# Kernel tuning notes

Measured on AMD Instinct MI355X. Metric: run time of the kernel, lower is better.

Reference implementation:

```python
import jax, jax.numpy as jnp
import numpy as np

B, L, D, H = 2, 2048, 1024, 16
DK = D // H


def setup_inputs() -> dict:
    key = jax.random.key(0)
    ks = jax.random.split(key, 5)
    s = 1.0 / np.sqrt(D)
    query = jax.random.normal(ks[0], (B, L, D), dtype=jnp.float32)
    # causal mask, True = masked (masked_fill semantics), broadcastable to [B,H,L,L]
    mask = jnp.triu(jnp.ones((L, L), dtype=bool), k=1)[None, None, :, :]
    W_q = jax.random.normal(ks[1], (D, D), dtype=jnp.float32) * s
    W_k = jax.random.normal(ks[2], (D, D), dtype=jnp.float32) * s
    W_v = jax.random.normal(ks[3], (D, D), dtype=jnp.float32) * s
    W_o = jax.random.normal(ks[4], (D, D), dtype=jnp.float32) * s
    return {"query": query, "mask": mask, "W_q": W_q, "W_k": W_k, "W_v": W_v, "W_o": W_o}


def reference(query, mask, W_q, W_k, W_v, W_o):
    b, l, d = query.shape
    # projections (torch Linear with bias=False; weights here stored as [in,out])
    q = (query @ W_q).reshape(b, l, H, DK).transpose(0, 2, 1, 3)  # [B,H,L,dk]
    k = (query @ W_k).reshape(b, l, H, DK).transpose(0, 2, 1, 3)
    v = (query @ W_v).reshape(b, l, H, DK).transpose(0, 2, 1, 3)
    scores = jnp.einsum("bhqd,bhkd->bhqk", q, k) / np.sqrt(DK)  # [B,H,L,L]
    scores = jnp.where(mask, jnp.asarray(-1e9, scores.dtype), scores)
    A = jax.nn.softmax(scores, axis=-1)  # [B,H,L,L]
    out = jnp.einsum("bhqk,bhkd->bhqd", A, v)  # [B,H,L,dk]
    out = out.transpose(0, 2, 1, 3).reshape(b, l, d)  # [B,L,D]
    y = out @ W_o
    return (y, A)
```

## Files before the change

kernel.cpp:

```cpp
#include <hip/hip_runtime.h>


typedef _Float16 h8 __attribute__((ext_vector_type(8)));
typedef _Float16 h4 __attribute__((ext_vector_type(4)));
typedef float f4 __attribute__((ext_vector_type(4)));

#define L_SEQ 2048
#define NH 16
#define DKH 64
#define DM 1024

static __device__ __forceinline__ void gload16(const void* g, void* l) {
  __builtin_amdgcn_global_load_lds(
      (const __attribute__((address_space(1))) char*)g,
      (__attribute__((address_space(3))) char*)l, 16, 0, 0);
}

__global__ __launch_bounds__(256) void k_cast(const float* __restrict__ in,
                                              _Float16* __restrict__ out, int n4) {
  int i = blockIdx.x * 256 + threadIdx.x;
  if (i >= n4) return;
  f4 v = ((const f4*)in)[i];
  h4 o = {(_Float16)v[0], (_Float16)v[1], (_Float16)v[2], (_Float16)v[3]};
  ((h4*)out)[i] = o;
}

__global__ __launch_bounds__(256) void k_wt(const float* w0, const float* w1,
                                            const float* w2, const float* w3,
                                            _Float16* o0, _Float16* o1,
                                            _Float16* o2, _Float16* o3) {
  __shared__ _Float16 tile[64][65];
  const float* W;
  _Float16* O;
  switch (blockIdx.z) {
    case 0: W = w0; O = o0; break;
    case 1: W = w1; O = o1; break;
    case 2: W = w2; O = o2; break;
    default: W = w3; O = o3; break;
  }
  int n0 = blockIdx.x * 64, k0 = blockIdx.y * 64;
  int t = threadIdx.x, c = t & 63, r0 = (t >> 6) * 16;
  for (int i = 0; i < 16; ++i)
    tile[r0 + i][c] = (_Float16)W[(size_t)(k0 + r0 + i) * DM + n0 + c];
  __syncthreads();
  for (int i = 0; i < 16; ++i)
    O[(size_t)(n0 + r0 + i) * DM + k0 + c] = tile[c][r0 + i];
}

__global__ __launch_bounds__(256) void k_vt(const _Float16* __restrict__ Vb,
                                            _Float16* __restrict__ Vt) {
  __shared__ _Float16 tile[64][65];
  int blk = blockIdx.x, bh = blk >> 5, l0 = (blk & 31) * 64;
  const _Float16* src = Vb + (size_t)bh * L_SEQ * DKH;
  _Float16* dst = Vt + (size_t)bh * DKH * L_SEQ;
  int t = threadIdx.x, c = t & 63, r0 = (t >> 6) * 16;
  for (int i = 0; i < 16; ++i)
    tile[r0 + i][c] = src[(size_t)(l0 + r0 + i) * DKH + c];
  __syncthreads();
  for (int i = 0; i < 16; ++i)
    dst[(size_t)(r0 + i) * L_SEQ + l0 + c] = tile[c][r0 + i];
}

__global__ __launch_bounds__(256) void k_gemm(const _Float16* __restrict__ A,
                                              const _Float16* __restrict__ B0,
                                              const _Float16* __restrict__ B1,
                                              const _Float16* __restrict__ B2,
                                              void* o0, void* o1, void* o2,
                                              int mode) {
  const _Float16* Bt = blockIdx.z == 0 ? B0 : (blockIdx.z == 1 ? B1 : B2);
  void* out = blockIdx.z == 0 ? o0 : (blockIdx.z == 1 ? o1 : o2);
  __shared__ __align__(16) _Float16 lA[128 * 32];
  __shared__ __align__(16) _Float16 lB[128 * 32];
  int t = threadIdx.x, lane = t & 63, w = t >> 6;
  int l15 = lane & 15, g = lane >> 4;
  int wr = w >> 1, wc = w & 1;
  int m0 = blockIdx.x * 128, n0 = blockIdx.y * 128;
  f4 zed = {0.f, 0.f, 0.f, 0.f};
  f4 acc[4][4];
  for (int i = 0; i < 4; ++i)
    for (int j = 0; j < 4; ++j) acc[i][j] = zed;

  int row = t >> 2, colh = (t & 3) * 8;
  const _Float16* ga = A + (size_t)(m0 + row) * DM + colh;
  const _Float16* gb = Bt + (size_t)(n0 + row) * DM + colh;
  _Float16* la0 = &lA[row * 32 + colh];
  _Float16* la1 = &lA[2048 + row * 32 + colh];
  _Float16* lb0 = &lB[row * 32 + colh];
  _Float16* lb1 = &lB[2048 + row * 32 + colh];

  for (int k0 = 0; k0 < DM; k0 += 32) {
    __syncthreads();
    gload16(ga + k0, la0);
    gload16(ga + (size_t)64 * DM + k0, la1);
    gload16(gb + k0, lb0);
    gload16(gb + (size_t)64 * DM + k0, lb1);
    __syncthreads();
    h8 af[4], bfr[4];
#pragma unroll
    for (int mr = 0; mr < 4; ++mr)
      af[mr] = *(const h8*)&lA[(wr * 64 + mr * 16 + l15) * 32 + g * 8];
#pragma unroll
    for (int nr = 0; nr < 4; ++nr)
      bfr[nr] = *(const h8*)&lB[(wc * 64 + nr * 16 + l15) * 32 + g * 8];
#pragma unroll
    for (int mr = 0; mr < 4; ++mr)
#pragma unroll
      for (int nr = 0; nr < 4; ++nr)
        acc[mr][nr] = __builtin_amdgcn_mfma_f32_16x16x32_f16(af[mr], bfr[nr],
                                                             acc[mr][nr], 0, 0, 0);
  }

  if (mode == 0) {
    _Float16* o = (_Float16*)out;
#pragma unroll
    for (int mr = 0; mr < 4; ++mr)
#pragma unroll
      for (int nr = 0; nr < 4; ++nr) {
        int n = n0 + wc * 64 + nr * 16 + l15;
        int h = n >> 6, dk = n & 63;
#pragma unroll
        for (int r = 0; r < 4; ++r) {
          int m = m0 + wr * 64 + mr * 16 + g * 4 + r;
          int b = m >> 11, l = m & 2047;
          o[(((size_t)b * NH + h) * L_SEQ + l) * DKH + dk] = (_Float16)acc[mr][nr][r];
        }
      }
  } else {
    float* o = (float*)out;
#pragma unroll
    for (int mr = 0; mr < 4; ++mr)
#pragma unroll
      for (int nr = 0; nr < 4; ++nr) {
        int n = n0 + wc * 64 + nr * 16 + l15;
#pragma unroll
        for (int r = 0; r < 4; ++r) {
          int m = m0 + wr * 64 + mr * 16 + g * 4 + r;
          o[(size_t)m * DM + n] = acc[mr][nr][r];
        }
      }
  }
}

__global__ __launch_bounds__(256, 2) void k_attn(const _Float16* __restrict__ Qh,
                                                 const _Float16* __restrict__ Kh,
                                                 const _Float16* __restrict__ Vt,
                                                 float* __restrict__ Aout,
                                                 _Float16* __restrict__ Oh) {
  __shared__ __align__(16) _Float16 Plds[4][2][1024];
  const int blk = blockIdx.x;
  const int bh = blk & 31;
  const int qt = 15 - (blk >> 5);
  const int b = bh >> 4, h = bh & 15;
  const int t = threadIdx.x, w = t >> 6, lane = t & 63;
  const int l15 = lane & 15, g = lane >> 4;
  const int q0 = qt * 128 + w * 32;
  const int qa = q0 + l15;
  const int qb = q0 + 16 + l15;

  const _Float16* Qp = Qh + ((size_t)bh * L_SEQ + qa) * DKH + g * 8;
  const h8 qa0 = *(const h8*)Qp;
  const h8 qa1 = *(const h8*)(Qp + 32);
  const h8 qb0 = *(const h8*)(Qp + 16 * DKH);
  const h8 qb1 = *(const h8*)(Qp + 16 * DKH + 32);
  const _Float16* Kbase = Kh + (size_t)bh * L_SEQ * DKH;
  const _Float16* Vbase = Vt + (size_t)bh * DKH * L_SEQ;
  float* Abase = Aout + (size_t)bh * L_SEQ * L_SEQ;
  char* pA = (char*)&Plds[w][0][0];
  char* pB = (char*)&Plds[w][1][0];
  const int swz = (l15 & 7) << 4;

  const float SC = 0.125f * 1.44269504089f;
  const int nfull = q0 >> 6;
  f4 zed = {0.f, 0.f, 0.f, 0.f};

  float mA = -1e30f, sumA = 0.f, mB = -1e30f, sumB = 0.f;
  for (int c = 0; c < nfull; ++c) {
    const _Float16* Kp = Kbase + (size_t)(c * 64 + l15) * DKH + g * 8;
    h8 kf0[4], kf1[4];
#pragma unroll
    for (int tt = 0; tt < 4; ++tt) {
      kf0[tt] = *(const h8*)(Kp + (size_t)tt * 16 * DKH);
      kf1[tt] = *(const h8*)(Kp + (size_t)tt * 16 * DKH + 32);
    }
    f4 sa[4], sb[4];
    __builtin_amdgcn_s_setprio(1);
#pragma unroll
    for (int tt = 0; tt < 4; ++tt) {
      sa[tt] = __builtin_amdgcn_mfma_f32_16x16x32_f16(kf0[tt], qa0, zed, 0, 0, 0);
      sa[tt] = __builtin_amdgcn_mfma_f32_16x16x32_f16(kf1[tt], qa1, sa[tt], 0, 0, 0);
      sb[tt] = __builtin_amdgcn_mfma_f32_16x16x32_f16(kf0[tt], qb0, zed, 0, 0, 0);
      sb[tt] = __builtin_amdgcn_mfma_f32_16x16x32_f16(kf1[tt], qb1, sb[tt], 0, 0, 0);
    }
    __builtin_amdgcn_s_setprio(0);
#pragma unroll
    for (int tt = 0; tt < 4; ++tt)
#pragma unroll
      for (int r = 0; r < 4; ++r) {
        float va = sa[tt][r] * SC, vb = sb[tt][r] * SC;
        mA = fmaxf(mA, va);
        sumA += __builtin_amdgcn_exp2f(va);
        mB = fmaxf(mB, vb);
        sumB += __builtin_amdgcn_exp2f(vb);
      }
  }
  {
    const _Float16* Kp = Kbase + (size_t)(nfull * 64 + l15) * DKH + g * 8;
    h8 kf0[4], kf1[4];
#pragma unroll
    for (int tt = 0; tt < 4; ++tt) {
      kf0[tt] = *(const h8*)(Kp + (size_t)tt * 16 * DKH);
      kf1[tt] = *(const h8*)(Kp + (size_t)tt * 16 * DKH + 32);
    }
    f4 sa[4], sb[4];
    __builtin_amdgcn_s_setprio(1);
#pragma unroll
    for (int tt = 0; tt < 4; ++tt) {
      sa[tt] = __builtin_amdgcn_mfma_f32_16x16x32_f16(kf0[tt], qa0, zed, 0, 0, 0);
      sa[tt] = __builtin_amdgcn_mfma_f32_16x16x32_f16(kf1[tt], qa1, sa[tt], 0, 0, 0);
      sb[tt] = __builtin_amdgcn_mfma_f32_16x16x32_f16(kf0[tt], qb0, zed, 0, 0, 0);
      sb[tt] = __builtin_amdgcn_mfma_f32_16x16x32_f16(kf1[tt], qb1, sb[tt], 0, 0, 0);
    }
    __builtin_amdgcn_s_setprio(0);
#pragma unroll
    for (int tt = 0; tt < 4; ++tt) {
      int kb = nfull * 64 + tt * 16 + g * 4;
#pragma unroll
      for (int r = 0; r < 4; ++r) {
        float va = (kb + r <= qa) ? sa[tt][r] * SC : -1e30f;
        float vb = (kb + r <= qb) ? sb[tt][r] * SC : -1e30f;
        mA = fmaxf(mA, va);
        sumA += __builtin_amdgcn_exp2f(va);
        mB = fmaxf(mB, vb);
        sumB += __builtin_amdgcn_exp2f(vb);
      }
    }
  }
  mA = fmaxf(mA, __shfl_xor(mA, 16, 64));
  sumA += __shfl_xor(sumA, 16, 64);
  mA = fmaxf(mA, __shfl_xor(mA, 32, 64));
  sumA += __shfl_xor(sumA, 32, 64);
  mB = fmaxf(mB, __shfl_xor(mB, 16, 64));
  sumB += __shfl_xor(sumB, 16, 64);
  mB = fmaxf(mB, __shfl_xor(mB, 32, 64));
  sumB += __shfl_xor(sumB, 32, 64);
  const float cA = fmaxf(mA - 12.f, 0.f);
  const float cB = fmaxf(mB - 12.f, 0.f);
  const float invA = __builtin_amdgcn_exp2f(cA) / sumA;
  const float invB = __builtin_amdgcn_exp2f(cB) / sumB;

  f4 oaccA[4], oaccB[4];
#pragma unroll
  for (int dt = 0; dt < 4; ++dt) { oaccA[dt] = zed; oaccB[dt] = zed; }

  for (int cc = 0; cc <= nfull; ++cc) {
    const _Float16* Kp = Kbase + (size_t)(cc * 64 + l15) * DKH + g * 8;
    h8 kf0[4], kf1[4];
#pragma unroll
    for (int tt = 0; tt < 4; ++tt) {
      kf0[tt] = *(const h8*)(Kp + (size_t)tt * 16 * DKH);
      kf1[tt] = *(const h8*)(Kp + (size_t)tt * 16 * DKH + 32);
    }
    const _Float16* Vp = Vbase + (size_t)l15 * L_SEQ + cc * 64 + g * 8;
    h8 vf[8];
#pragma unroll
    for (int ks = 0; ks < 2; ++ks)
#pragma unroll
      for (int dt = 0; dt < 4; ++dt)
        vf[ks * 4 + dt] = *(const h8*)(Vp + (size_t)dt * 16 * L_SEQ + ks * 32);

    f4 sa[4], sb[4];
    __builtin_amdgcn_s_setprio(1);
#pragma unroll
    for (int tt = 0; tt < 4; ++tt) {
      sa[tt] = __builtin_amdgcn_mfma_f32_16x16x32_f16(kf0[tt], qa0, zed, 0, 0, 0);
      sa[tt] = __builtin_amdgcn_mfma_f32_16x16x32_f16(kf1[tt], qa1, sa[tt], 0, 0, 0);
      sb[tt] = __builtin_amdgcn_mfma_f32_16x16x32_f16(kf0[tt], qb0, zed, 0, 0, 0);
      sb[tt] = __builtin_amdgcn_mfma_f32_16x16x32_f16(kf1[tt], qb1, sb[tt], 0, 0, 0);
    }
    __builtin_amdgcn_s_setprio(0);

    const bool dchunk = (cc == nfull);
    float* ArowA = Abase + (size_t)qa * L_SEQ + cc * 64 + g * 4;
    float* ArowB = Abase + (size_t)qb * L_SEQ + cc * 64 + g * 4;
#pragma unroll
    for (int tt = 0; tt < 4; ++tt) {
      f4 pv;
#pragma unroll
      for (int r = 0; r < 4; ++r) {
        float sv = sa[tt][r] * SC - cA;
        if (dchunk && (cc * 64 + tt * 16 + g * 4 + r > qa)) sv = -1e30f;
        pv[r] = __builtin_amdgcn_exp2f(sv);
      }
      f4 av = {pv[0] * invA, pv[1] * invA, pv[2] * invA, pv[3] * invA};
      *(f4*)(ArowA + tt * 16) = av;
      h4 ph = {(_Float16)pv[0], (_Float16)pv[1], (_Float16)pv[2], (_Float16)pv[3]};
      *(h4*)(pA + l15 * 128 + ((tt * 32 + g * 8) ^ swz)) = ph;
    }
#pragma unroll
    for (int tt = 0; tt < 4; ++tt) {
      f4 pv;
#pragma unroll
      for (int r = 0; r < 4; ++r) {
        float sv = sb[tt][r] * SC - cB;
        if (dchunk && (cc * 64 + tt * 16 + g * 4 + r > qb)) sv = -1e30f;
        pv[r] = __builtin_amdgcn_exp2f(sv);
      }
      f4 av = {pv[0] * invB, pv[1] * invB, pv[2] * invB, pv[3] * invB};
      *(f4*)(ArowB + tt * 16) = av;
      h4 ph = {(_Float16)pv[0], (_Float16)pv[1], (_Float16)pv[2], (_Float16)pv[3]};
      *(h4*)(pB + l15 * 128 + ((tt * 32 + g * 8) ^ swz)) = ph;
    }
    asm volatile("s_waitcnt lgkmcnt(0)" ::: "memory");
    __builtin_amdgcn_sched_barrier(0);
    __builtin_amdgcn_s_setprio(1);
#pragma unroll
    for (int ks = 0; ks < 2; ++ks) {
      h8 pfa = *(const h8*)(pA + l15 * 128 + ((ks * 64 + g * 16) ^ swz));
      h8 pfb = *(const h8*)(pB + l15 * 128 + ((ks * 64 + g * 16) ^ swz));
#pragma unroll
      for (int dt = 0; dt < 4; ++dt) {
        oaccA[dt] = __builtin_amdgcn_mfma_f32_16x16x32_f16(pfa, vf[ks * 4 + dt],
                                                           oaccA[dt], 0, 0, 0);
        oaccB[dt] = __builtin_amdgcn_mfma_f32_16x16x32_f16(pfb, vf[ks * 4 + dt],
                                                           oaccB[dt], 0, 0, 0);
      }
    }
    __builtin_amdgcn_s_setprio(0);
  }

  float scA[4], scB[4];
#pragma unroll
  for (int r = 0; r < 4; ++r) {
    scA[r] = __shfl(invA, g * 4 + r, 64);
    scB[r] = __shfl(invB, g * 4 + r, 64);
  }
#pragma unroll
  for (int dt = 0; dt < 4; ++dt)
#pragma unroll
    for (int r = 0; r < 4; ++r) {
      int qra = q0 + g * 4 + r;
      Oh[((size_t)b * L_SEQ + qra) * DM + h * DKH + dt * 16 + l15] =
          (_Float16)(oaccA[dt][r] * scA[r]);
      Oh[((size_t)b * L_SEQ + qra + 16) * DM + h * DKH + dt * 16 + l15] =
          (_Float16)(oaccB[dt][r] * scB[r]);
    }

  const int zs = (nfull + 1) * 64;
  for (int rr = 0; rr < 32; ++rr) {
    float* p = Abase + (size_t)(q0 + rr) * L_SEQ;
    for (int cz = zs + lane * 4; cz < L_SEQ; cz += 256)
      *(f4*)(p + cz) = zed;
  }
}

extern "C" void kernel_launch(void* const* d_in, const int* in_sizes, int n_in,
                              void* d_out, int out_size, void* d_ws, size_t ws_size,
                              hipStream_t stream) {
  const float* query = (const float*)d_in[0];
  const float* Wq = (const float*)d_in[2];
  const float* Wk = (const float*)d_in[3];
  const float* Wv = (const float*)d_in[4];
  const float* Wo = (const float*)d_in[5];

  char* ws = (char*)d_ws;
  _Float16* qh  = (_Float16*)(ws);
  _Float16* Wtq = (_Float16*)(ws + (8ull  << 20));
  _Float16* Wtk = (_Float16*)(ws + (10ull << 20));
  _Float16* Wtv = (_Float16*)(ws + (12ull << 20));
  _Float16* Wto = (_Float16*)(ws + (14ull << 20));
  _Float16* Qh  = (_Float16*)(ws + (16ull << 20));
  _Float16* Kh  = (_Float16*)(ws + (24ull << 20));
  _Float16* Vh  = (_Float16*)(ws + (32ull << 20));
  _Float16* Vtr = (_Float16*)(ws + (40ull << 20));
  _Float16* Oh  = (_Float16*)(ws + (48ull << 20));

  float* y = (float*)d_out;
  float* Afull = y + (size_t)4194304;

  k_cast<<<4096, 256, 0, stream>>>(query, qh, 1048576);
  k_wt<<<dim3(16, 16, 4), 256, 0, stream>>>(Wq, Wk, Wv, Wo, Wtq, Wtk, Wtv, Wto);
  k_gemm<<<dim3(32, 8, 3), 256, 0, stream>>>(qh, Wtq, Wtk, Wtv, Qh, Kh, Vh, 0);
  k_vt<<<1024, 256, 0, stream>>>(Vh, Vtr);
  k_attn<<<512, 256, 0, stream>>>(Qh, Kh, Vtr, Afull, Oh);
  k_gemm<<<dim3(32, 8, 1), 256, 0, stream>>>(Oh, Wto, Wto, Wto, y, y, y, 1);
}
```

Measured before the change: 286.8 us.

## Double-buffer K loads, fold softmax scale into Wq, reorder tiles, nontemporal A stores

Software-pipelines the K fragment loads in both attention passes so the next chunk's K is fetched while the current chunk's MFMAs and softmax run. It folds the 1/sqrt(dk)*log2(e) scale into the fp16 transposed W_q, which removes a per-element multiply in the score paths. Query-tile order changes so the second half of blocks runs short tiles in ascending order, balancing causal work across waves. Attention-matrix stores and zero-fill use nontemporal stores to reduce cache pollution. The cost is higher register pressure from the double-buffered K fragments, and pre-scaling W_q in fp16 changes rounding slightly.

```diff
diff --git a/kernel.cpp b/kernel.cpp
--- a/kernel.cpp
+++ b/kernel.cpp
@@ -38,10 +38,11 @@
     case 2: W = w2; O = o2; break;
     default: W = w3; O = o3; break;
   }
+  const float scl = (blockIdx.z == 0) ? 0.18033688011112042f : 1.0f;
   int n0 = blockIdx.x * 64, k0 = blockIdx.y * 64;
   int t = threadIdx.x, c = t & 63, r0 = (t >> 6) * 16;
   for (int i = 0; i < 16; ++i)
-    tile[r0 + i][c] = (_Float16)W[(size_t)(k0 + r0 + i) * DM + n0 + c];
+    tile[r0 + i][c] = (_Float16)(W[(size_t)(k0 + r0 + i) * DM + n0 + c] * scl);
   __syncthreads();
   for (int i = 0; i < 16; ++i)
     O[(size_t)(n0 + r0 + i) * DM + k0 + c] = tile[c][r0 + i];
@@ -149,7 +150,8 @@
   __shared__ __align__(16) _Float16 Plds[4][2][1024];
   const int blk = blockIdx.x;
   const int bh = blk & 31;
-  const int qt = 15 - (blk >> 5);
+  const int td = blk >> 5;
+  const int qt = (td < 8) ? (15 - td) : (td - 8);
   const int b = bh >> 4, h = bh & 15;
   const int t = threadIdx.x, w = t >> 6, lane = t & 63;
   const int l15 = lane & 15, g = lane >> 4;
@@ -169,70 +171,61 @@
   char* pB = (char*)&Plds[w][1][0];
   const int swz = (l15 & 7) << 4;
 
-  const float SC = 0.125f * 1.44269504089f;
   const int nfull = q0 >> 6;
   f4 zed = {0.f, 0.f, 0.f, 0.f};
 
+#define LOADK(F0, F1, CC)                                                  \
+  do {                                                                     \
+    const _Float16* Kp_ = Kbase + (size_t)((CC) * 64 + l15) * DKH + g * 8; \
+    _Pragma("unroll") for (int u = 0; u < 4; ++u) {                        \
+      F0[u] = *(const h8*)(Kp_ + (size_t)u * 16 * DKH);                    \
+      F1[u] = *(const h8*)(Kp_ + (size_t)u * 16 * DKH + 32);               \
+    }                                                                      \
+  } while (0)
+
+#define QKMM(F0, F1)                                                          \
+  do {                                                                        \
+    __builtin_amdgcn_s_setprio(1);                                            \
+    _Pragma("unroll") for (int u = 0; u < 4; ++u) {                           \
+      sa[u] = __builtin_amdgcn_mfma_f32_16x16x32_f16(F0[u], qa0, zed, 0, 0, 0); \
+      sa[u] = __builtin_amdgcn_mfma_f32_16x16x32_f16(F1[u], qa1, sa[u], 0, 0, 0); \
+      sb[u] = __builtin_amdgcn_mfma_f32_16x16x32_f16(F0[u], qb0, zed, 0, 0, 0); \
+      sb[u] = __builtin_amdgcn_mfma_f32_16x16x32_f16(F1[u], qb1, sb[u], 0, 0, 0); \
+    }                                                                         \
+    __builtin_amdgcn_s_setprio(0);                                            \
+  } while (0)
+
   float mA = -1e30f, sumA = 0.f, mB = -1e30f, sumB = 0.f;
-  for (int c = 0; c < nfull; ++c) {
-    const _Float16* Kp = Kbase + (size_t)(c * 64 + l15) * DKH + g * 8;
-    h8 kf0[4], kf1[4];
-#pragma unroll
-    for (int tt = 0; tt < 4; ++tt) {
-      kf0[tt] = *(const h8*)(Kp + (size_t)tt * 16 * DKH);
-      kf1[tt] = *(const h8*)(Kp + (size_t)tt * 16 * DKH + 32);
-    }
+#define P1ACC(CC)                                                         \
+  do {                                                                    \
+    const bool dg_ = ((CC) == nfull);                                     \
+    _Pragma("unroll") for (int u = 0; u < 4; ++u) {                       \
+      int kb_ = (CC) * 64 + u * 16 + g * 4;                               \
+      _Pragma("unroll") for (int r = 0; r < 4; ++r) {                     \
+        float va = (!dg_ || kb_ + r <= qa) ? sa[u][r] : -1e30f;           \
+        float vb = (!dg_ || kb_ + r <= qb) ? sb[u][r] : -1e30f;           \
+        mA = fmaxf(mA, va);                                               \
+        sumA += __builtin_amdgcn_exp2f(va);                               \
+        mB = fmaxf(mB, vb);                                               \
+        sumB += __builtin_amdgcn_exp2f(vb);                               \
+      }                                                                   \
+    }                                                                     \
+  } while (0)
+  {
+    h8 ka0[4], ka1[4], kb0[4], kb1[4];
     f4 sa[4], sb[4];
-    __builtin_amdgcn_s_setprio(1);
-#pragma unroll
-    for (int tt = 0; tt < 4; ++tt) {
-      sa[tt] = __builtin_amdgcn_mfma_f32_16x16x32_f16(kf0[tt], qa0, zed, 0, 0, 0);
-      sa[tt] = __builtin_amdgcn_mfma_f32_16x16x32_f16(kf1[tt], qa1, sa[tt], 0, 0, 0);
-      sb[tt] = __builtin_amdgcn_mfma_f32_16x16x32_f16(kf0[tt], qb0, zed, 0, 0, 0);
-      sb[tt] = __builtin_amdgcn_mfma_f32_16x16x32_f16(kf1[tt], qb1, sb[tt], 0, 0, 0);
-    }
-    __builtin_amdgcn_s_setprio(0);
-#pragma unroll
-    for (int tt = 0; tt < 4; ++tt)
-#pragma unroll
-      for (int r = 0; r < 4; ++r) {
-        float va = sa[tt][r] * SC, vb = sb[tt][r] * SC;
-        mA = fmaxf(mA, va);
-        sumA += __builtin_amdgcn_exp2f(va);
-        mB = fmaxf(mB, vb);
-        sumB += __builtin_amdgcn_exp2f(vb);
-      }
-  }
-  {
-    const _Float16* Kp = Kbase + (size_t)(nfull * 64 + l15) * DKH + g * 8;
-    h8 kf0[4], kf1[4];
-#pragma unroll
-    for (int tt = 0; tt < 4; ++tt) {
-      kf0[tt] = *(const h8*)(Kp + (size_t)tt * 16 * DKH);
-      kf1[tt] = *(const h8*)(Kp + (size_t)tt * 16 * DKH + 32);
-    }
-    f4 sa[4], sb[4];
-    __builtin_amdgcn_s_setprio(1);
-#pragma unroll
-    for (int tt = 0; tt < 4; ++tt) {
-      sa[tt] = __builtin_amdgcn_mfma_f32_16x16x32_f16(kf0[tt], qa0, zed, 0, 0, 0);
-      sa[tt] = __builtin_amdgcn_mfma_f32_16x16x32_f16(kf1[tt], qa1, sa[tt], 0, 0, 0);
-      sb[tt] = __builtin_amdgcn_mfma_f32_16x16x32_f16(kf0[tt], qb0, zed, 0, 0, 0);
-      sb[tt] = __builtin_amdgcn_mfma_f32_16x16x32_f16(kf1[tt], qb1, sb[tt], 0, 0, 0);
-    }
-    __builtin_amdgcn_s_setprio(0);
-#pragma unroll
-    for (int tt = 0; tt < 4; ++tt) {
-      int kb = nfull * 64 + tt * 16 + g * 4;
-#pragma unroll
-      for (int r = 0; r < 4; ++r) {
-        float va = (kb + r <= qa) ? sa[tt][r] * SC : -1e30f;
-        float vb = (kb + r <= qb) ? sb[tt][r] * SC : -1e30f;
-        mA = fmaxf(mA, va);
-        sumA += __builtin_amdgcn_exp2f(va);
-        mB = fmaxf(mB, vb);
-        sumB += __builtin_amdgcn_exp2f(vb);
-      }
+    LOADK(ka0, ka1, 0);
+    int cc = 0;
+    while (true) {
+      if (cc + 1 <= nfull) LOADK(kb0, kb1, cc + 1);
+      QKMM(ka0, ka1);
+      P1ACC(cc);
+      if (cc + 1 > nfull) break;
+      if (cc + 2 <= nfull) LOADK(ka0, ka1, cc + 2);
+      QKMM(kb0, kb1);
+      P1ACC(cc + 1);
+      if (cc + 2 > nfull) break;
+      cc += 2;
     }
   }
   mA = fmaxf(mA, __shfl_xor(mA, 16, 64));
@@ -252,80 +245,72 @@
 #pragma unroll
   for (int dt = 0; dt < 4; ++dt) { oaccA[dt] = zed; oaccB[dt] = zed; }
 
-  for (int cc = 0; cc <= nfull; ++cc) {
-    const _Float16* Kp = Kbase + (size_t)(cc * 64 + l15) * DKH + g * 8;
-    h8 kf0[4], kf1[4];
-#pragma unroll
-    for (int tt = 0; tt < 4; ++tt) {
-      kf0[tt] = *(const h8*)(Kp + (size_t)tt * 16 * DKH);
-      kf1[tt] = *(const h8*)(Kp + (size_t)tt * 16 * DKH + 32);
+#define P2STEP(F0, F1, CC)                                                    \
+  do {                                                                        \
+    const bool dg_ = ((CC) == nfull);                                         \
+    const _Float16* Vp_ = Vbase + (size_t)l15 * L_SEQ + (CC) * 64 + g * 8;    \
+    h8 vf[8];                                                                 \
+    _Pragma("unroll") for (int ks = 0; ks < 2; ++ks)                          \
+        _Pragma("unroll") for (int dt = 0; dt < 4; ++dt)                      \
+            vf[ks * 4 + dt] =                                                 \
+                *(const h8*)(Vp_ + (size_t)dt * 16 * L_SEQ + ks * 32);        \
+    QKMM(F0, F1);                                                             \
+    float* ArowA = Abase + (size_t)qa * L_SEQ + (CC) * 64 + g * 4;            \
+    float* ArowB = Abase + (size_t)qb * L_SEQ + (CC) * 64 + g * 4;            \
+    _Pragma("unroll") for (int u = 0; u < 4; ++u) {                           \
+      f4 pva, pvb;                                                            \
+      _Pragma("unroll") for (int r = 0; r < 4; ++r) {                         \
+        float sva = sa[u][r] - cA;                                            \
+        float svb = sb[u][r] - cB;                                            \
+        if (dg_) {                                                            \
+          int kk_ = (CC) * 64 + u * 16 + g * 4 + r;                           \
+          if (kk_ > qa) sva = -1e30f;                                         \
+          if (kk_ > qb) svb = -1e30f;                                         \
+        }                                                                     \
+        pva[r] = __builtin_amdgcn_exp2f(sva);                                 \
+        pvb[r] = __builtin_amdgcn_exp2f(svb);                                 \
+      }                                                                       \
+      f4 ava = {pva[0] * invA, pva[1] * invA, pva[2] * invA, pva[3] * invA};  \
+      f4 avb = {pvb[0] * invB, pvb[1] * invB, pvb[2] * invB, pvb[3] * invB};  \
+      __builtin_nontemporal_store(ava, (f4*)(ArowA + u * 16));                \
+      __builtin_nontemporal_store(avb, (f4*)(ArowB + u * 16));                \
+      h4 pha = {(_Float16)pva[0], (_Float16)pva[1], (_Float16)pva[2],         \
+                (_Float16)pva[3]};                                            \
+      h4 phb = {(_Float16)pvb[0], (_Float16)pvb[1], (_Float16)pvb[2],         \
+                (_Float16)pvb[3]};                                            \
+      *(h4*)(pA + l15 * 128 + ((u * 32 + g * 8) ^ swz)) = pha;                \
+      *(h4*)(pB + l15 * 128 + ((u * 32 + g * 8) ^ swz)) = phb;                \
+    }                                                                         \
+    asm volatile("s_waitcnt lgkmcnt(0)" ::: "memory");                        \
+    __builtin_amdgcn_sched_barrier(0);                                        \
+    __builtin_amdgcn_s_setprio(1);                                            \
+    _Pragma("unroll") for (int ks = 0; ks < 2; ++ks) {                        \
+      h8 pfa = *(const h8*)(pA + l15 * 128 + ((ks * 64 + g * 16) ^ swz));     \
+      h8 pfb = *(const h8*)(pB + l15 * 128 + ((ks * 64 + g * 16) ^ swz));     \
+      _Pragma("unroll") for (int dt = 0; dt < 4; ++dt) {                      \
+        oaccA[dt] = __builtin_amdgcn_mfma_f32_16x16x32_f16(                   \
+            pfa, vf[ks * 4 + dt], oaccA[dt], 0, 0, 0);                        \
+        oaccB[dt] = __builtin_amdgcn_mfma_f32_16x16x32_f16(                   \
+            pfb, vf[ks * 4 + dt], oaccB[dt], 0, 0, 0);                        \
+      }                                                                       \
+    }                                                                         \
+    __builtin_amdgcn_s_setprio(0);                                            \
+  } while (0)
+
+  {
+    h8 ka0[4], ka1[4], kb0[4], kb1[4];
+    f4 sa[4], sb[4];
+    LOADK(ka0, ka1, 0);
+    int cc = 0;
+    while (true) {
+      if (cc + 1 <= nfull) LOADK(kb0, kb1, cc + 1);
+      P2STEP(ka0, ka1, cc);
+      if (cc + 1 > nfull) break;
+      if (cc + 2 <= nfull) LOADK(ka0, ka1, cc + 2);
+      P2STEP(kb0, kb1, cc + 1);
+      if (cc + 2 > nfull) break;
+      cc += 2;
     }
-    const _Float16* Vp = Vbase + (size_t)l15 * L_SEQ + cc * 64 + g * 8;
-    h8 vf[8];
-#pragma unroll
-    for (int ks = 0; ks < 2; ++ks)
-#pragma unroll
-      for (int dt = 0; dt < 4; ++dt)
-        vf[ks * 4 + dt] = *(const h8*)(Vp + (size_t)dt * 16 * L_SEQ + ks * 32);
-
-    f4 sa[4], sb[4];
-    __builtin_amdgcn_s_setprio(1);
-#pragma unroll
-    for (int tt = 0; tt < 4; ++tt) {
-      sa[tt] = __builtin_amdgcn_mfma_f32_16x16x32_f16(kf0[tt], qa0, zed, 0, 0, 0);
-      sa[tt] = __builtin_amdgcn_mfma_f32_16x16x32_f16(kf1[tt], qa1, sa[tt], 0, 0, 0);
-      sb[tt] = __builtin_amdgcn_mfma_f32_16x16x32_f16(kf0[tt], qb0, zed, 0, 0, 0);
-      sb[tt] = __builtin_amdgcn_mfma_f32_16x16x32_f16(kf1[tt], qb1, sb[tt], 0, 0, 0);
-    }
-    __builtin_amdgcn_s_setprio(0);
-
-    const bool dchunk = (cc == nfull);
-    float* ArowA = Abase + (size_t)qa * L_SEQ + cc * 64 + g * 4;
-    float* ArowB = Abase + (size_t)qb * L_SEQ + cc * 64 + g * 4;
-#pragma unroll
-    for (int tt = 0; tt < 4; ++tt) {
-      f4 pv;
-#pragma unroll
-      for (int r = 0; r < 4; ++r) {
-        float sv = sa[tt][r] * SC - cA;
-        if (dchunk && (cc * 64 + tt * 16 + g * 4 + r > qa)) sv = -1e30f;
-        pv[r] = __builtin_amdgcn_exp2f(sv);
-      }
-      f4 av = {pv[0] * invA, pv[1] * invA, pv[2] * invA, pv[3] * invA};
-      *(f4*)(ArowA + tt * 16) = av;
-      h4 ph = {(_Float16)pv[0], (_Float16)pv[1], (_Float16)pv[2], (_Float16)pv[3]};
-      *(h4*)(pA + l15 * 128 + ((tt * 32 + g * 8) ^ swz)) = ph;
-    }
-#pragma unroll
-    for (int tt = 0; tt < 4; ++tt) {
-      f4 pv;
-#pragma unroll
-      for (int r = 0; r < 4; ++r) {
-        float sv = sb[tt][r] * SC - cB;
-        if (dchunk && (cc * 64 + tt * 16 + g * 4 + r > qb)) sv = -1e30f;
-        pv[r] = __builtin_amdgcn_exp2f(sv);
-      }
-      f4 av = {pv[0] * invB, pv[1] * invB, pv[2] * invB, pv[3] * invB};
-      *(f4*)(ArowB + tt * 16) = av;
-      h4 ph = {(_Float16)pv[0], (_Float16)pv[1], (_Float16)pv[2], (_Float16)pv[3]};
-      *(h4*)(pB + l15 * 128 + ((tt * 32 + g * 8) ^ swz)) = ph;
-    }
-    asm volatile("s_waitcnt lgkmcnt(0)" ::: "memory");
-    __builtin_amdgcn_sched_barrier(0);
-    __builtin_amdgcn_s_setprio(1);
-#pragma unroll
-    for (int ks = 0; ks < 2; ++ks) {
-      h8 pfa = *(const h8*)(pA + l15 * 128 + ((ks * 64 + g * 16) ^ swz));
-      h8 pfb = *(const h8*)(pB + l15 * 128 + ((ks * 64 + g * 16) ^ swz));
-#pragma unroll
-      for (int dt = 0; dt < 4; ++dt) {
-        oaccA[dt] = __builtin_amdgcn_mfma_f32_16x16x32_f16(pfa, vf[ks * 4 + dt],
-                                                           oaccA[dt], 0, 0, 0);
-        oaccB[dt] = __builtin_amdgcn_mfma_f32_16x16x32_f16(pfb, vf[ks * 4 + dt],
-                                                           oaccB[dt], 0, 0, 0);
-      }
-    }
-    __builtin_amdgcn_s_setprio(0);
   }
 
   float scA[4], scB[4];
@@ -338,10 +323,9 @@
   for (int dt = 0; dt < 4; ++dt)
 #pragma unroll
     for (int r = 0; r < 4; ++r) {
-      int qra = q0 + g * 4 + r;
-      Oh[((size_t)b * L_SEQ + qra) * DM + h * DKH + dt * 16 + l15] =
+      Oh[((size_t)b * L_SEQ + q0 + g * 4 + r) * DM + h * DKH + dt * 16 + l15] =
           (_Float16)(oaccA[dt][r] * scA[r]);
-      Oh[((size_t)b * L_SEQ + qra + 16) * DM + h * DKH + dt * 16 + l15] =
+      Oh[((size_t)b * L_SEQ + q0 + 16 + g * 4 + r) * DM + h * DKH + dt * 16 + l15] =
           (_Float16)(oaccB[dt][r] * scB[r]);
     }
 
@@ -349,7 +333,7 @@
   for (int rr = 0; rr < 32; ++rr) {
     float* p = Abase + (size_t)(q0 + rr) * L_SEQ;
     for (int cz = zs + lane * 4; cz < L_SEQ; cz += 256)
-      *(f4*)(p + cz) = zed;
+      __builtin_nontemporal_store(zed, (f4*)(p + cz));
   }
 }
 
```

Result: slower. 314.4 us (+9.6%).
